# Kernel tuning notes

Measured on AMD Instinct MI355X. Metric: run time of the kernel, lower is better.

Reference implementation:

```python
import jax, jax.numpy as jnp
import numpy as np

N, E, DIN, HID, G, L = 50000, 200000, 128, 128, 64, 6
H1, H2 = 8, 4
EPS_LN, EPS_BN = 1e-5, 1e-5


def setup_inputs() -> dict:
    key = jax.random.key(0)
    ks = iter(jax.random.split(key, 32))
    def nrm(shape, scale=0.05):
        return jax.random.normal(next(ks), shape, dtype=jnp.float32) * scale
    z = lambda *s: jnp.zeros(s, jnp.float32)
    o = lambda *s: jnp.ones(s, jnp.float32)
    return {
        'x': jax.random.normal(next(ks), (N, DIN), dtype=jnp.float32),
        'edge_index': jax.random.randint(next(ks), (2, E), 0, N),
        'batch': jnp.sort(jax.random.randint(next(ks), (N,), 0, G)),
        'W1': nrm((DIN, H1 * HID)), 'a_src1': nrm((H1, HID)), 'a_dst1': nrm((H1, HID)), 'b1': z(H1 * HID),
        'W2': nrm((H1 * HID, H2 * HID)), 'a_src2': nrm((H2, HID)), 'a_dst2': nrm((H2, HID)), 'b2': z(H2 * HID),
        'W3': nrm((H2 * HID, HID)), 'b3': z(HID),
        'wq': nrm((L, HID, HID)), 'bq': z(L, HID), 'wk': nrm((L, HID, HID)), 'bk': z(L, HID),
        'wv': nrm((L, HID, HID)), 'bv': z(L, HID), 'wo': nrm((L, HID, HID)), 'bo': z(L, HID),
        'ln1g': o(L, HID), 'ln1b': z(L, HID), 'ln2g': o(L, HID), 'ln2b': z(L, HID),
        'wf1': nrm((L, HID, 4 * HID)), 'bf1': z(L, 4 * HID), 'wf2': nrm((L, 4 * HID, HID)), 'bf2': z(L, HID),
        'bn1_g': o(2 * HID), 'bn1_b': z(2 * HID),
        'fc1_w': nrm((2 * HID, HID // 2)), 'fc1_b': z(HID // 2),
        'bn2_g': o(HID // 2), 'bn2_b': z(HID // 2),
        'fc2_w': nrm((HID // 2, 2)), 'fc2_b': z(2),
    }


def _ln(x, g, b):
    mu = x.mean(-1, keepdims=True)
    v = ((x - mu) ** 2).mean(-1, keepdims=True)
    return (x - mu) * jax.lax.rsqrt(v + EPS_LN) * g + b


def _gat(x, src, dst, W, a_s, a_d, b, heads):
    # PyG GATConv: message src -> dst, segment softmax over incoming edges per dst.
    h = (x @ W).reshape(x.shape[0], heads, -1)           # [N, H, C]
    e = jax.nn.leaky_relu((h * a_s).sum(-1)[src] + (h * a_d).sum(-1)[dst], 0.2)  # [E, H]
    m = jax.ops.segment_max(e, dst, num_segments=N)
    ex = jnp.exp(e - jnp.where(jnp.isfinite(m), m, 0.0)[dst])
    s = jax.ops.segment_sum(ex, dst, num_segments=N)
    alpha = ex / (s[dst] + 1e-16)
    out = jax.ops.segment_sum(alpha[:, :, None] * h[src], dst, num_segments=N)
    return out.reshape(N, -1) + b


def _forward(x, edge_index, batch, W1, a_src1, a_dst1, b1, W2, a_src2, a_dst2, b2, W3, b3,
             wq, bq, wk, bk, wv, bv, wo, bo, ln1g, ln1b, ln2g, ln2b, wf1, bf1, wf2, bf2,
             bn1_g, bn1_b, fc1_w, fc1_b, bn2_g, bn2_b, fc2_w, fc2_b):
    loop = jnp.arange(N, dtype=edge_index.dtype)
    src = jnp.concatenate([edge_index[0], loop])          # add self-loops (PyG default)
    dst = jnp.concatenate([edge_index[1], loop])
    h = jax.nn.elu(_gat(x, src, dst, W1, a_src1, a_dst1, b1, H1))
    h = jax.nn.elu(_gat(h, src, dst, W2, a_src2, a_dst2, b2, H2))
    # GCNConv with symmetric normalization (self-loops already included)
    deg = jax.ops.segment_sum(jnp.ones(src.shape, h.dtype), dst, num_segments=N)
    dinv = jnp.where(deg > 0, jax.lax.rsqrt(jnp.maximum(deg, 1e-12)), 0.0)
    norm = dinv[src] * dinv[dst]
    h = jax.nn.elu(jax.ops.segment_sum(norm[:, None] * (h @ W3)[src], dst, num_segments=N) + b3)
    # TransformerEncoder over seq_len=1 (h3.unsqueeze(1)): softmax over one key == 1,
    # so MHA output == Wo @ (Wv h + bv) + bo exactly; q/k have no effect on the output.
    for l in range(L):
        sa = (h @ wv[l] + bv[l]) @ wo[l] + bo[l]
        h = _ln(h + sa, ln1g[l], ln1b[l])
        ff = jax.nn.gelu(h @ wf1[l] + bf1[l], approximate=False) @ wf2[l] + bf2[l]
        h = _ln(h + ff, ln2g[l], ln2b[l])
    # global mean / max pool over graphs
    cnt = jax.ops.segment_sum(jnp.ones((N,), h.dtype), batch, num_segments=G)
    hm = jax.ops.segment_sum(h, batch, num_segments=G) / jnp.maximum(cnt, 1.0)[:, None]
    hx = jax.ops.segment_max(h, batch, num_segments=G)
    hx = jnp.where(jnp.isfinite(hx), hx, 0.0)
    hc = jnp.concatenate([hm, hx], axis=1)                # [G, 2*HID]
    bn_s = 1.0 / np.sqrt(1.0 + EPS_BN)                    # eval BN: running stats (0, 1)
    hc = hc * bn_s * bn1_g + bn1_b
    hc = jax.nn.elu(hc @ fc1_w + fc1_b)
    hc = hc * bn_s * bn2_g + bn2_b
    return hc @ fc2_w + fc2_b                             # [G, 2]


def reference(x, edge_index, batch, W1, a_src1, a_dst1, b1, W2, a_src2, a_dst2, b2, W3, b3,
              wq, bq, wk, bk, wv, bv, wo, bo, ln1g, ln1b, ln2g, ln2b, wf1, bf1, wf2, bf2,
              bn1_g, bn1_b, fc1_w, fc1_b, bn2_g, bn2_b, fc2_w, fc2_b):
    return _forward(x, edge_index, batch, W1, a_src1, a_dst1, b1, W2, a_src2, a_dst2, b2, W3, b3,
                    wq, bq, wk, bk, wv, bv, wo, bo, ln1g, ln1b, ln2g, ln2b, wf1, bf1, wf2, bf2,
                    bn1_g, bn1_b, fc1_w, fc1_b, bn2_g, bn2_b, fc2_w, fc2_b)
```

## Files before the change

kernel.cpp:

```cpp
#include <hip/hip_runtime.h>
#include <hip/hip_bf16.h>
#include <math.h>

#define NN 50000
#define EE 200000
#define ET 250000
#define GG 64
#define LL 6

using short8 = __attribute__((ext_vector_type(8))) short;
using f32x4  = __attribute__((ext_vector_type(4))) float;
typedef unsigned short ushortT;

__device__ __forceinline__ float elu1(float x) { return x > 0.f ? x : expm1f(x); }
__device__ __forceinline__ float gelu_exact(float x) {
    return 0.5f * x * (1.f + erff(x * 0.70710678118654752440f));
}
__device__ __forceinline__ short f2bf(float f) {
    __hip_bfloat16 h = __float2bfloat16(f);
    return *reinterpret_cast<short*>(&h);
}
__device__ __forceinline__ float bf2f(ushortT u) {
    return __uint_as_float(((unsigned)u) << 16);
}
__device__ __forceinline__ void accum8(float* acc, float a, uint4 d) {
    acc[0] += a * bf2f((ushortT)(d.x & 0xffff));
    acc[1] += a * bf2f((ushortT)(d.x >> 16));
    acc[2] += a * bf2f((ushortT)(d.y & 0xffff));
    acc[3] += a * bf2f((ushortT)(d.y >> 16));
    acc[4] += a * bf2f((ushortT)(d.z & 0xffff));
    acc[5] += a * bf2f((ushortT)(d.z >> 16));
    acc[6] += a * bf2f((ushortT)(d.w & 0xffff));
    acc[7] += a * bf2f((ushortT)(d.w >> 16));
}

__global__ void count_deg_kernel(const int* __restrict__ ei, int* __restrict__ deg) {
    int e = blockIdx.x * 256 + threadIdx.x;
    if (e >= ET) return;
    int dst = (e < EE) ? ei[EE + e] : (e - EE);
    atomicAdd(&deg[dst], 1);
}

__global__ void scan_kernel(const int* __restrict__ deg, int* __restrict__ row_ptr, int n) {
    __shared__ int s[1024];
    int tid = threadIdx.x;
    const int per = (n + 1023) / 1024;
    int lo = tid * per, hi = min(lo + per, n);
    int sum = 0;
    for (int i = lo; i < hi; i++) sum += deg[i];
    s[tid] = sum;
    __syncthreads();
    for (int off = 1; off < 1024; off <<= 1) {
        int t = (tid >= off) ? s[tid - off] : 0;
        __syncthreads();
        s[tid] += t;
        __syncthreads();
    }
    int run = s[tid] - sum;
    for (int i = lo; i < hi; i++) { row_ptr[i] = run; run += deg[i]; }
    if (tid == 1023) row_ptr[n] = s[1023];
}

__global__ void fill_csr_kernel(const int* __restrict__ ei, const int* __restrict__ row_ptr,
                                int* __restrict__ cursor, int* __restrict__ edge_src) {
    int e = blockIdx.x * 256 + threadIdx.x;
    if (e >= ET) return;
    int src, dst;
    if (e < EE) { src = ei[e]; dst = ei[EE + e]; }
    else        { src = e - EE; dst = e - EE; }
    int pos = atomicAdd(&cursor[dst], 1);
    edge_src[row_ptr[dst] + pos] = src;
}

__global__ void dinv_kernel(const int* __restrict__ row_ptr, float* __restrict__ dinv) {
    int n = blockIdx.x * 256 + threadIdx.x;
    if (n >= NN) return;
    int d = row_ptr[n + 1] - row_ptr[n];
    dinv[n] = (d > 0) ? rsqrtf((float)d) : 0.f;
}

__global__ __launch_bounds__(256) void local_sort_kernel(
    const int* __restrict__ row_ptr, int* __restrict__ perm, int n_nodes) {
    int g = blockIdx.x * 4 + (threadIdx.x >> 6);
    int l = threadIdx.x & 63;
    int node = g * 64 + l;
    if (g * 64 >= n_nodes) return;
    int d = (node < n_nodes) ? (row_ptr[node + 1] - row_ptr[node]) : 0x7fffffff;
    int rank = 0;
#pragma unroll 16
    for (int j = 0; j < 64; j++) {
        int dj = __shfl(d, j);
        rank += (dj < d) || (dj == d && j < l);
    }
    if (node < n_nodes) perm[g * 64 + rank] = node;
}

__global__ void wvwo_kernel(const float* __restrict__ wv, const float* __restrict__ wo,
                            const float* __restrict__ bv, const float* __restrict__ bo,
                            float* __restrict__ Wvo, float* __restrict__ bvo) {
    int l = blockIdx.y;
    const float* Wv = wv + l * 16384;
    const float* Wo = wo + l * 16384;
    int tid = blockIdx.x * 256 + threadIdx.x;
    if (tid < 16384) {
        int r = tid >> 7, c = tid & 127;
        float s = 0.f;
        for (int k = 0; k < 128; k++) s += Wv[r * 128 + k] * Wo[k * 128 + c];
        Wvo[l * 16384 + tid] = s;
    }
    if (blockIdx.x == 0 && threadIdx.x < 128) {
        int c = threadIdx.x;
        float s = bo[l * 128 + c];
        for (int k = 0; k < 128; k++) s += bv[l * 128 + k] * Wo[k * 128 + c];
        bvo[l * 128 + c] = s;
    }
}

__global__ void bprep_kernel(const float* __restrict__ B, short* __restrict__ Bp,
                             int K, int N, int ldb, long srcStride) {
    int layer = blockIdx.y;
    const float* Bsrc = B + srcStride * layer;
    short* Bd = Bp + (size_t)K * N * layer;
    int total = (K >> 5) * (N >> 4) * 64;
    int tid = blockIdx.x * 256 + threadIdx.x;
    if (tid >= total) return;
    int l = tid & 63;
    int rest = tid >> 6;
    int kbc = K >> 5;
    int kb = rest % kbc;
    int c16 = rest / kbc;
    int n = c16 * 16 + (l & 15);
    int kbase = kb * 32 + (l >> 4) * 8;
    short v[8];
#pragma unroll
    for (int j = 0; j < 8; j++) v[j] = f2bf(Bsrc[(size_t)(kbase + j) * ldb + n]);
    *(uint4*)(Bd + (size_t)tid * 8) = *(uint4*)v;
}

__global__ void cast_bf16_kernel(const float* __restrict__ in, short* __restrict__ out, int n4) {
    int i = blockIdx.x * 256 + threadIdx.x;
    if (i >= n4) return;
    float4 v = *(const float4*)(in + (size_t)i * 4);
    short s[4] = { f2bf(v.x), f2bf(v.y), f2bf(v.z), f2bf(v.w) };
    *(uint2*)(out + (size_t)i * 4) = *(uint2*)s;
}

template <int EPI, bool BIAS, bool OUTBF16, int NSPLIT, int KBC,
          bool TMAJ = false, bool ATILE32 = false>
__global__ __launch_bounds__(256) void gemm_bf16_kernel(
    const short* __restrict__ A, const short* __restrict__ Bp,
    const float* __restrict__ bias, void* __restrict__ Cv,
    const float* __restrict__ a_s, const float* __restrict__ a_d,
    float* __restrict__ as_out, float* __restrict__ ad_out, int asH,
    const ushortT* __restrict__ Rres, const float* __restrict__ lng,
    const float* __restrict__ lnb, float* __restrict__ Qout,
    __hip_bfloat16* __restrict__ Qbout,
    int M, int K, int Nc) {
    __shared__ short Bs[(KBC > 0) ? KBC * 4096 : 8192];
    int t = threadIdx.x;
    int w = t >> 6, l = t & 63;
    int ln = l & 15, lq = l >> 4;
    int MBceil = (M + 63) >> 6;
    int bx = blockIdx.x;
    int xcd = bx & 7, idx = bx >> 3;
    int t2 = idx % NSPLIT;
    int mb = (idx / NSPLIT) * 8 + xcd;
    if (mb >= MBceil) return;
    int bm = mb * 64 + w * 16;
    int arow = bm + ln;
    bool aok = arow < M;
    int rowb = bm + lq * 4;
    const short* Ap = A + (size_t)arow * K + lq * 8;

    auto aload = [&](int kb) -> short8 {
        if (!aok) return (short8){0, 0, 0, 0, 0, 0, 0, 0};
        const short* p;
        if constexpr (ATILE32)
            p = A + ((size_t)kb * M + arow) * 32 + lq * 8;
        else
            p = Ap + kb * 32;
        return *(const short8*)p;
    };

    f32x4 acc[8];
#pragma unroll
    for (int j = 0; j < 8; j++) acc[j] = (f32x4){0.f, 0.f, 0.f, 0.f};

    if constexpr (KBC > 0) {
        {
            const uint4* src = (const uint4*)(Bp + (size_t)t2 * KBC * 4096);
            uint4* dst = (uint4*)Bs;
#pragma unroll
            for (int i = 0; i < KBC * 2; i++)
                dst[i * 256 + t] = src[i * 256 + t];
        }
        short8 af[KBC];
#pragma unroll
        for (int kb = 0; kb < KBC; kb++)
            af[kb] = aload(kb);
        __syncthreads();
#pragma unroll
        for (int kb = 0; kb < KBC; kb++)
#pragma unroll
            for (int ct = 0; ct < 8; ct++) {
                short8 bfr = *(const short8*)(Bs + ((ct * KBC + kb) * 64 + l) * 8);
                acc[ct] = __builtin_amdgcn_mfma_f32_16x16x32_bf16(af[kb], bfr, acc[ct], 0, 0, 0);
            }
    } else {
        int kbc = K >> 5;
        int sct = t >> 5, spart = t & 31;
        auto stage = [&](int buf, int kb) {
            const uint4* src = (const uint4*)(Bp + ((size_t)(t2 * 8 + sct) * kbc + kb) * 512);
            uint4* dst = (uint4*)(Bs + buf * 4096 + sct * 512);
            dst[spart * 2]     = src[spart * 2];
            dst[spart * 2 + 1] = src[spart * 2 + 1];
        };
        stage(0, 0);
        __syncthreads();
        for (int kb = 0; kb < kbc; kb++) {
            if (kb + 1 < kbc) stage((kb + 1) & 1, kb + 1);
            short8 af = aload(kb);
            const short* bsb = Bs + (kb & 1) * 4096;
#pragma unroll
            for (int ct = 0; ct < 8; ct++) {
                short8 bfr = *(const short8*)(bsb + (ct * 64 + l) * 8);
                acc[ct] = __builtin_amdgcn_mfma_f32_16x16x32_bf16(af, bfr, acc[ct], 0, 0, 0);
            }
            __syncthreads();
        }
    }

    if (EPI == 2) {
        const float* asv = a_s + t2 * 128;
        const float* adv = a_d + t2 * 128;
#pragma unroll
        for (int reg = 0; reg < 4; reg++) {
            float vs = 0.f, vd = 0.f;
#pragma unroll
            for (int ct = 0; ct < 8; ct++) {
                int colL = ct * 16 + ln;
                float av = acc[ct][reg];
                vs += av * asv[colL];
                vd += av * adv[colL];
            }
            vs += __shfl_xor(vs, 1); vs += __shfl_xor(vs, 2);
            vs += __shfl_xor(vs, 4); vs += __shfl_xor(vs, 8);
            vd += __shfl_xor(vd, 1); vd += __shfl_xor(vd, 2);
            vd += __shfl_xor(vd, 4); vd += __shfl_xor(vd, 8);
            int row = rowb + reg;
            if (ln == 0 && row < M) {
                as_out[(size_t)row * asH + t2] = vs;
                ad_out[(size_t)row * asH + t2] = vd;
            }
        }
    }
    if (EPI == 3) {
        float v[8][4];
#pragma unroll
        for (int ct = 0; ct < 8; ct++) {
            int col = ct * 16 + ln;
            float bv_ = bias[col];
#pragma unroll
            for (int reg = 0; reg < 4; reg++) {
                int row = rowb + reg;
                float r = (row < M) ? bf2f(Rres[(size_t)row * 128 + col]) : 0.f;
                v[ct][reg] = acc[ct][reg] + bv_ + r;
            }
        }
#pragma unroll
        for (int reg = 0; reg < 4; reg++) {
            float s = 0.f;
#pragma unroll
            for (int ct = 0; ct < 8; ct++) s += v[ct][reg];
            s += __shfl_xor(s, 1); s += __shfl_xor(s, 2);
            s += __shfl_xor(s, 4); s += __shfl_xor(s, 8);
            float mean = s * (1.f / 128.f);
            float s2 = 0.f;
#pragma unroll
            for (int ct = 0; ct < 8; ct++) { float d = v[ct][reg] - mean; s2 += d * d; }
            s2 += __shfl_xor(s2, 1); s2 += __shfl_xor(s2, 2);
            s2 += __shfl_xor(s2, 4); s2 += __shfl_xor(s2, 8);
            float rstd = rsqrtf(s2 * (1.f / 128.f) + 1e-5f);
            int row = rowb + reg;
            if (row < M) {
#pragma unroll
                for (int ct = 0; ct < 8; ct++) {
                    int col = ct * 16 + ln;
                    float o = (v[ct][reg] - mean) * rstd * lng[col] + lnb[col];
                    Qbout[(size_t)row * 128 + col] = __float2bfloat16(o);
                    if (Qout) Qout[(size_t)row * 128 + col] = o;
                }
            }
        }
    }
    if (EPI == 0 || EPI == 1 || EPI == 2) {
#pragma unroll
        for (int ct = 0; ct < 8; ct++) {
            int col = t2 * 128 + ct * 16 + ln;
            float bv_ = BIAS ? bias[col] : 0.f;
#pragma unroll
            for (int reg = 0; reg < 4; reg++) {
                int row = rowb + reg;
                if (row < M) {
                    float v = acc[ct][reg] + bv_;
                    if (EPI == 1) v = gelu_exact(v);
                    if (OUTBF16) {
                        size_t addr;
                        if constexpr (TMAJ)
                            addr = ((size_t)(col >> 5) * M + row) * 32 + (col & 31);
                        else
                            addr = (size_t)row * Nc + col;
                        ((__hip_bfloat16*)Cv)[addr] = __float2bfloat16(v);
                    } else {
                        ((float*)Cv)[(size_t)row * Nc + col] = v;
                    }
                }
            }
        }
    }
}

__global__ __launch_bounds__(256) void ff_fused_kernel(
    const short* __restrict__ Qb, const short* __restrict__ wf1p,
    const short* __restrict__ wf2p, const float* __restrict__ bf1,
    const float* __restrict__ bf2, const float* __restrict__ lng,
    const float* __restrict__ lnb, float* __restrict__ Qout,
    __hip_bfloat16* __restrict__ Qbout, int M) {
    __shared__ short Bs[16384];
    __shared__ short Ts[4][16 * 132];
    int t = threadIdx.x;
    int w = t >> 6, l = t & 63;
    int ln = l & 15, lq = l >> 4;
    int MBceil = (M + 63) >> 6;
    int bx = blockIdx.x;
    int xcd = bx & 7, mb = (bx >> 3) * 8 + xcd;
    if (mb >= MBceil) return;
    int bm = mb * 64 + w * 16;
    int arow = bm + ln;
    bool aok = arow < M;
    int rowb = bm + lq * 4;

    short8 af1[4];
#pragma unroll
    for (int kb = 0; kb < 4; kb++)
        af1[kb] = aok ? *(const short8*)(Qb + (size_t)arow * 128 + kb * 32 + lq * 8)
                      : (short8){0, 0, 0, 0, 0, 0, 0, 0};

    f32x4 acc2[8];
#pragma unroll
    for (int j = 0; j < 8; j++) acc2[j] = (f32x4){0.f, 0.f, 0.f, 0.f};

    short* Tw = &Ts[w][0];
    for (int kc = 0; kc < 4; kc++) {
        __syncthreads();
        {
            const uint4* src = (const uint4*)(wf1p + kc * 16384);
            uint4* dst = (uint4*)Bs;
#pragma unroll
            for (int i = 0; i < 8; i++) dst[i * 256 + t] = src[i * 256 + t];
        }
        __syncthreads();
        f32x4 acct[8];
#pragma unroll
        for (int j = 0; j < 8; j++) acct[j] = (f32x4){0.f, 0.f, 0.f, 0.f};
#pragma unroll
        for (int kb = 0; kb < 4; kb++)
#pragma unroll
            for (int ct = 0; ct < 8; ct++) {
                short8 bfr = *(const short8*)(Bs + ((ct * 4 + kb) * 64 + l) * 8);
                acct[ct] = __builtin_amdgcn_mfma_f32_16x16x32_bf16(af1[kb], bfr, acct[ct], 0, 0, 0);
            }
#pragma unroll
        for (int ct = 0; ct < 8; ct++) {
            float bv = bf1[kc * 128 + ct * 16 + ln];
#pragma unroll
            for (int reg = 0; reg < 4; reg++)
                Tw[(lq * 4 + reg) * 132 + ct * 16 + ln] = f2bf(gelu_exact(acct[ct][reg] + bv));
        }
        __syncthreads();
        {
            int sct = t >> 5, spart = t & 31;
            const uint4* src = (const uint4*)(wf2p + (size_t)(sct * 16 + kc * 4) * 512);
            uint4* dst = (uint4*)Bs + sct * 256;
#pragma unroll
            for (int j = 0; j < 8; j++) dst[spart + j * 32] = src[spart + j * 32];
        }
        short8 a2[4];
#pragma unroll
        for (int kb2 = 0; kb2 < 4; kb2++)
            a2[kb2] = *(const short8*)(Tw + ln * 132 + kb2 * 32 + lq * 8);
        __syncthreads();
#pragma unroll
        for (int kb2 = 0; kb2 < 4; kb2++)
#pragma unroll
            for (int ct = 0; ct < 8; ct++) {
                short8 bfr = *(const short8*)(Bs + ((ct * 4 + kb2) * 64 + l) * 8);
                acc2[ct] = __builtin_amdgcn_mfma_f32_16x16x32_bf16(a2[kb2], bfr, acc2[ct], 0, 0, 0);
            }
    }

    float v[8][4];
#pragma unroll
    for (int ct = 0; ct < 8; ct++) {
        int col = ct * 16 + ln;
        float bv_ = bf2[col];
#pragma unroll
        for (int reg = 0; reg < 4; reg++) {
            int row = rowb + reg;
            float r = (row < M) ? bf2f(((const ushortT*)Qb)[(size_t)row * 128 + col]) : 0.f;
            v[ct][reg] = acc2[ct][reg] + bv_ + r;
        }
    }
#pragma unroll
    for (int reg = 0; reg < 4; reg++) {
        float s = 0.f;
#pragma unroll
        for (int ct = 0; ct < 8; ct++) s += v[ct][reg];
        s += __shfl_xor(s, 1); s += __shfl_xor(s, 2);
        s += __shfl_xor(s, 4); s += __shfl_xor(s, 8);
        float mean = s * (1.f / 128.f);
        float s2 = 0.f;
#pragma unroll
        for (int ct = 0; ct < 8; ct++) { float d = v[ct][reg] - mean; s2 += d * d; }
        s2 += __shfl_xor(s2, 1); s2 += __shfl_xor(s2, 2);
        s2 += __shfl_xor(s2, 4); s2 += __shfl_xor(s2, 8);
        float rstd = rsqrtf(s2 * (1.f / 128.f) + 1e-5f);
        int row = rowb + reg;
        if (row < M) {
#pragma unroll
            for (int ct = 0; ct < 8; ct++) {
                int col = ct * 16 + ln;
                float o = (v[ct][reg] - mean) * rstd * lng[col] + lnb[col];
                Qbout[(size_t)row * 128 + col] = __float2bfloat16(o);
                if (Qout) Qout[(size_t)row * 128 + col] = o;
            }
        }
    }
}

template <int H>
__global__ __launch_bounds__(256) void gat_alpha_kernel(
    const float* __restrict__ as_, const float* __restrict__ ad_,
    const int* __restrict__ row_ptr, const int* __restrict__ edge_src,
    float* __restrict__ exA, float* __restrict__ exS, int n_nodes) {
    const int GS = 64 / H;
    int node = blockIdx.x * 4 + (threadIdx.x >> 6);
    if (node >= n_nodes) return;
    int l = threadIdx.x & 63;
    int h = l / GS;
    int lig = l % GS;
    int start = row_ptr[node];
    int deg = row_ptr[node + 1] - start;
    float adn = ad_[(size_t)node * H + h];
    float m = -1e30f;
    for (int j = lig; j < deg; j += GS) {
        int s = edge_src[start + j];
        float e = as_[(size_t)s * H + h] + adn;
        e = e > 0.f ? e : 0.2f * e;
        m = fmaxf(m, e);
    }
#pragma unroll
    for (int mask = 1; mask < GS; mask <<= 1)
        m = fmaxf(m, __shfl_xor(m, mask));
    float S = 0.f;
    for (int j = lig; j < deg; j += GS) {
        int s = edge_src[start + j];
        float e = as_[(size_t)s * H + h] + adn;
        e = e > 0.f ? e : 0.2f * e;
        float ex = expf(e - m);
        exA[(size_t)h * ET + (start + j)] = ex;
        S += ex;
    }
#pragma unroll
    for (int mask = 1; mask < GS; mask <<= 1)
        S += __shfl_xor(S, mask);
    if (lig == 0) exS[(size_t)h * n_nodes + node] = S;
}

__global__ __launch_bounds__(256) void gat_agg_tiled_kernel(
    const ushortT* __restrict__ hT, const float* __restrict__ exA,
    const float* __restrict__ exS, const float* __restrict__ bias,
    const int* __restrict__ row_ptr, const int* __restrict__ edge_src,
    const int* __restrict__ perm,
    __hip_bfloat16* __restrict__ outT, int n_nodes, int NB) {
    int bx = blockIdx.x;
    int xcd = bx & 7, rest = bx >> 3;
    int tl = rest / NB, nb = rest - tl * NB;
    int tile = tl * 8 + xcd;
    int nl = threadIdx.x >> 2, q = threadIdx.x & 3;
    int idx = nb * 64 + nl;
    if (idx >= n_nodes) return;
    int node = perm[idx];
    int hb = tile >> 2;
    const ushortT* __restrict__ base = hT + (size_t)tile * n_nodes * 32 + q * 8;
    const float* __restrict__ exAh = exA + (size_t)hb * ET;
    int start = row_ptr[node];
    int deg = row_ptr[node + 1] - start;
    float acc[8];
#pragma unroll
    for (int c = 0; c < 8; c++) acc[c] = 0.f;
    for (int j = 0; j < deg; j++) {
        int s = edge_src[start + j];
        float a = exAh[start + j];
        uint4 d = *(const uint4*)(base + (size_t)s * 32);
        accum8(acc, a, d);
    }
    float inv = 1.f / (exS[(size_t)hb * n_nodes + node] + 1e-16f);
    const float* bp = bias + tile * 32 + q * 8;
    short o[8];
#pragma unroll
    for (int c = 0; c < 8; c++)
        o[c] = f2bf(elu1(acc[c] * inv + bp[c]));
    *(uint4*)(outT + ((size_t)tile * n_nodes + node) * 32 + q * 8) = *(uint4*)o;
}

__global__ __launch_bounds__(256, 2) void gcn_agg_kernel(
    const ushortT* __restrict__ hp, const float* __restrict__ dinv,
    const float* __restrict__ b3, const int* __restrict__ row_ptr,
    const int* __restrict__ edge_src,
    __hip_bfloat16* __restrict__ outb, int n_nodes) {
    int node = blockIdx.x * 2 + (threadIdx.x >> 7);
    int c = threadIdx.x & 127;
    if (node >= n_nodes) return;
    int start = row_ptr[node];
    int deg = row_ptr[node + 1] - start;
    float dn = dinv[node];
    float acc = 0.f;
    auto LS = [&](int j) { return edge_src[start + min(j, deg - 1)]; };
    int s0 = LS(0), s1 = LS(1), s2 = LS(2), s3 = LS(3);
    int s4 = LS(4), s5 = LS(5), s6 = LS(6), s7 = LS(7);
    auto HW = [&](int s, int j, float& h, float& w) {
        h = bf2f(hp[(size_t)s * 128 + c]);
        w = (j < deg) ? dinv[s] * dn : 0.f;
    };
    float h0, h1, h2, h3, h4, h5, h6, h7;
    float w0, w1, w2, w3, w4, w5, w6, w7;
    HW(s0, 0, h0, w0); HW(s1, 1, h1, w1); HW(s2, 2, h2, w2); HW(s3, 3, h3, w3);
    HW(s4, 4, h4, w4); HW(s5, 5, h5, w5); HW(s6, 6, h6, w6); HW(s7, 7, h7, w7);
    int j0 = 0;
    while (true) {
        int jn = j0 + 8;
        bool more = jn < deg;
        float g0, g1, g2, g3, g4, g5, g6, g7;
        float v0 = 0.f, v1 = 0.f, v2 = 0.f, v3 = 0.f;
        float v4 = 0.f, v5 = 0.f, v6 = 0.f, v7 = 0.f;
        if (more) {
            int t0 = LS(jn),     t1 = LS(jn + 1), t2 = LS(jn + 2), t3 = LS(jn + 3);
            int t4 = LS(jn + 4), t5 = LS(jn + 5), t6 = LS(jn + 6), t7 = LS(jn + 7);
            HW(t0, jn,     g0, v0); HW(t1, jn + 1, g1, v1);
            HW(t2, jn + 2, g2, v2); HW(t3, jn + 3, g3, v3);
            HW(t4, jn + 4, g4, v4); HW(t5, jn + 5, g5, v5);
            HW(t6, jn + 6, g6, v6); HW(t7, jn + 7, g7, v7);
        }
        acc += w0 * h0 + w1 * h1 + w2 * h2 + w3 * h3
             + w4 * h4 + w5 * h5 + w6 * h6 + w7 * h7;
        if (!more) break;
        h0 = g0; h1 = g1; h2 = g2; h3 = g3;
        h4 = g4; h5 = g5; h6 = g6; h7 = g7;
        w0 = v0; w1 = v1; w2 = v2; w3 = v3;
        w4 = v4; w5 = v5; w6 = v6; w7 = v7;
        j0 = jn;
    }
    outb[(size_t)node * 128 + c] = __float2bfloat16(elu1(acc + b3[c]));
}

__global__ void pool1_kernel(const float* __restrict__ Q, const int* __restrict__ batch,
                             float* __restrict__ psum, float* __restrict__ pmax, int n_nodes) {
    int g = blockIdx.x, seg = blockIdx.y;
    int c = threadIdx.x;
    int lo, hi;
    {
        int l = 0, h = n_nodes;
        while (l < h) { int mid = (l + h) >> 1; if (batch[mid] < g) l = mid + 1; else h = mid; }
        lo = l;
        l = lo; h = n_nodes;
        while (l < h) { int mid = (l + h) >> 1; if (batch[mid] < g + 1) l = mid + 1; else h = mid; }
        hi = l;
    }
    int len = hi - lo;
    int a = lo + (int)((long)len * seg / 8);
    int b = lo + (int)((long)len * (seg + 1) / 8);
    float s = 0.f, mx = -INFINITY;
    for (int n = a; n < b; n++) {
        float v = Q[(size_t)n * 128 + c];
        s += v;
        mx = fmaxf(mx, v);
    }
    psum[(g * 8 + seg) * 128 + c] = s;
    pmax[(g * 8 + seg) * 128 + c] = mx;
}

__global__ void pool2_kernel(const float* __restrict__ psum, const float* __restrict__ pmax,
                             const int* __restrict__ batch,
                             const float* __restrict__ bn1g, const float* __restrict__ bn1b,
                             float* __restrict__ hc, int n_nodes) {
    int g = blockIdx.x;
    int c = threadIdx.x;
    int lo, hi;
    {
        int l = 0, h = n_nodes;
        while (l < h) { int mid = (l + h) >> 1; if (batch[mid] < g) l = mid + 1; else h = mid; }
        lo = l;
        l = lo; h = n_nodes;
        while (l < h) { int mid = (l + h) >> 1; if (batch[mid] < g + 1) l = mid + 1; else h = mid; }
        hi = l;
    }
    int cnt = hi - lo;
    float s = 0.f, mx = -INFINITY;
    for (int seg = 0; seg < 8; seg++) {
        s += psum[(g * 8 + seg) * 128 + c];
        mx = fmaxf(mx, pmax[(g * 8 + seg) * 128 + c]);
    }
    float hm = s / fmaxf((float)cnt, 1.f);
    float hx = (cnt > 0 && isfinite(mx)) ? mx : 0.f;
    const float bn_s = 0.99999500003749968f;
    hc[g * 256 + c]       = hm * bn_s * bn1g[c] + bn1b[c];
    hc[g * 256 + 128 + c] = hx * bn_s * bn1g[128 + c] + bn1b[128 + c];
}

__global__ void head_kernel(const float* __restrict__ hc,
                            const float* __restrict__ fc1w, const float* __restrict__ fc1b,
                            const float* __restrict__ bn2g, const float* __restrict__ bn2b,
                            const float* __restrict__ fc2w, const float* __restrict__ fc2b,
                            float* __restrict__ out) {
    int g = blockIdx.x;
    int j = threadIdx.x;
    const float bn_s = 0.99999500003749968f;
    float acc = fc1b[j];
    for (int i = 0; i < 256; i++) acc += hc[g * 256 + i] * fc1w[i * 64 + j];
    acc = elu1(acc);
    acc = acc * bn_s * bn2g[j] + bn2b[j];
    __shared__ float sv[64];
    sv[j] = acc;
    __syncthreads();
    if (j < 2) {
        float o = fc2b[j];
        for (int i = 0; i < 64; i++) o += sv[i] * fc2w[i * 2 + j];
        out[g * 2 + j] = o;
    }
}

extern "C" void kernel_launch(void* const* d_in, const int* in_sizes, int n_in,
                              void* d_out, int out_size, void* d_ws, size_t ws_size,
                              hipStream_t stream) {
    const float* x    = (const float*)d_in[0];
    const int*   ei   = (const int*)d_in[1];
    const int*   batch= (const int*)d_in[2];
    const float* W1   = (const float*)d_in[3];
    const float* as1  = (const float*)d_in[4];
    const float* ad1  = (const float*)d_in[5];
    const float* b1   = (const float*)d_in[6];
    const float* W2   = (const float*)d_in[7];
    const float* as2  = (const float*)d_in[8];
    const float* ad2  = (const float*)d_in[9];
    const float* b2   = (const float*)d_in[10];
    const float* W3   = (const float*)d_in[11];
    const float* b3   = (const float*)d_in[12];
    const float* wv   = (const float*)d_in[17];
    const float* bv   = (const float*)d_in[18];
    const float* wo   = (const float*)d_in[19];
    const float* bo   = (const float*)d_in[20];
    const float* ln1g = (const float*)d_in[21];
    const float* ln1b = (const float*)d_in[22];
    const float* ln2g = (const float*)d_in[23];
    const float* ln2b = (const float*)d_in[24];
    const float* wf1  = (const float*)d_in[25];
    const float* bf1  = (const float*)d_in[26];
    const float* wf2  = (const float*)d_in[27];
    const float* bf2  = (const float*)d_in[28];
    const float* bn1g = (const float*)d_in[29];
    const float* bn1b = (const float*)d_in[30];
    const float* fc1w = (const float*)d_in[31];
    const float* fc1b = (const float*)d_in[32];
    const float* bn2g = (const float*)d_in[33];
    const float* bn2b = (const float*)d_in[34];
    const float* fc2w = (const float*)d_in[35];
    const float* fc2b = (const float*)d_in[36];
    float* out = (float*)d_out;

    char* wsb = (char*)d_ws;
    short* xb    = (short*)wsb;
    float* exAf  = (float*)wsb;
    float* exSf  = (float*)(wsb + 8000000);
    short* h1t   = (short*)(wsb + 12800000);
    short* h2t   = (short*)(wsb + 12800000);
    short* h3pre = (short*)(wsb + 12800000);
    short* bh1   = (short*)(wsb + 115200000);
    short* bh2   = (short*)(wsb + 115200000);
    float* fQ    = (float*)(wsb + 128000000);
    short* Qb    = (short*)(wsb + 153600000);
    char* tail = wsb + 217600000;
    short* W1p  = (short*)tail;  tail += 262144;
    short* W2p  = (short*)tail;  tail += 1048576;
    short* W3p  = (short*)tail;  tail += 131072;
    short* Wvop = (short*)tail;  tail += 196608;
    short* wf1p = (short*)tail;  tail += 786432;
    short* wf2p = (short*)tail;  tail += 786432;
    float* Wvo  = (float*)tail;  tail += 393216;
    float* bvo  = (float*)tail;  tail += 3072;
    float* fAS  = (float*)tail;  tail += 1600000;
    float* fAD  = (float*)tail;  tail += 1600000;
    float* fDv  = (float*)tail;  tail += 200000;
    float* psum = (float*)tail;  tail += 262144;
    float* pmax = (float*)tail;  tail += 262144;
    float* fHC  = (float*)tail;  tail += 65536;
    int* iDeg   = (int*)tail;    tail += 200000;
    int* iRP    = (int*)tail;    tail += 200004;
    int* iCur   = (int*)tail;    tail += 200000;
    int* iES    = (int*)tail;    tail += 1000000;

    hipMemsetAsync(iDeg, 0, NN * sizeof(int), stream);
    hipMemsetAsync(iCur, 0, NN * sizeof(int), stream);

    count_deg_kernel<<<(ET + 255) / 256, 256, 0, stream>>>(ei, iDeg);
    scan_kernel<<<1, 1024, 0, stream>>>(iDeg, iRP, NN);
    fill_csr_kernel<<<(ET + 255) / 256, 256, 0, stream>>>(ei, iRP, iCur, iES);
    dinv_kernel<<<(NN + 255) / 256, 256, 0, stream>>>(iRP, fDv);
    int* perm = iCur;
    local_sort_kernel<<<(NN / 64 + 4) / 4, 256, 0, stream>>>(iRP, perm, NN);

    wvwo_kernel<<<dim3(64, 6), 256, 0, stream>>>(wv, wo, bv, bo, Wvo, bvo);
    auto bprep = [&](const float* B, short* Bp, int K, int N, int ldb, long sStride, int layers) {
        int total = (K >> 5) * (N >> 4) * 64;
        dim3 grid((total + 255) / 256, layers);
        bprep_kernel<<<grid, 256, 0, stream>>>(B, Bp, K, N, ldb, sStride);
    };
    bprep(W1, W1p, 128, 1024, 1024, 0, 1);
    bprep(W2, W2p, 1024, 512, 512, 0, 1);
    bprep(W3, W3p, 512, 128, 128, 0, 1);
    bprep(Wvo, Wvop, 128, 128, 128, 16384, 6);
    bprep(wf1, wf1p, 128, 512, 512, 65536, 6);
    bprep(wf2, wf2p, 512, 128, 128, 65536, 6);
    cast_bf16_kernel<<<(NN * 128 / 4 + 255) / 256, 256, 0, stream>>>(x, xb, NN * 128 / 4);

    const int MB64 = (NN + 63) / 64;
    const int MBp = ((MB64 + 7) / 8) * 8;
    const int NB = (NN + 63) / 64;

    gemm_bf16_kernel<2, false, true, 8, 4, true, false><<<MBp * 8, 256, 0, stream>>>(
        xb, W1p, nullptr, h1t, as1, ad1, fAS, fAD, 8,
        nullptr, nullptr, nullptr, nullptr, nullptr, NN, 128, 1024);
    gat_alpha_kernel<8><<<(NN + 3) / 4, 256, 0, stream>>>(
        fAS, fAD, iRP, iES, exAf, exSf, NN);
    gat_agg_tiled_kernel<<<4 * NB * 8, 256, 0, stream>>>(
        (const ushortT*)h1t, exAf, exSf, b1, iRP, iES, perm, (__hip_bfloat16*)bh1, NN, NB);
    gemm_bf16_kernel<2, false, true, 4, 0, true, true><<<MBp * 4, 256, 0, stream>>>(
        bh1, W2p, nullptr, h2t, as2, ad2, fAS, fAD, 4,
        nullptr, nullptr, nullptr, nullptr, nullptr, NN, 1024, 512);
    gat_alpha_kernel<4><<<(NN + 3) / 4, 256, 0, stream>>>(
        fAS, fAD, iRP, iES, exAf, exSf, NN);
    gat_agg_tiled_kernel<<<2 * NB * 8, 256, 0, stream>>>(
        (const ushortT*)h2t, exAf, exSf, b2, iRP, iES, perm, (__hip_bfloat16*)bh2, NN, NB);
    gemm_bf16_kernel<0, false, true, 1, 0, false, true><<<MBp, 256, 0, stream>>>(
        bh2, W3p, nullptr, h3pre, nullptr, nullptr, nullptr, nullptr, 0,
        nullptr, nullptr, nullptr, nullptr, nullptr, NN, 512, 128);
    gcn_agg_kernel<<<(NN + 1) / 2, 256, 0, stream>>>(
        (const ushortT*)h3pre, fDv, b3, iRP, iES, (__hip_bfloat16*)Qb, NN);
    for (int l = 0; l < LL; l++) {
        gemm_bf16_kernel<3, true, false, 1, 4><<<MBp, 256, 0, stream>>>(
            Qb, Wvop + l * 16384, bvo + l * 128, nullptr, nullptr, nullptr, nullptr, nullptr, 0,
            (const ushortT*)Qb, ln1g + l * 128, ln1b + l * 128, nullptr, (__hip_bfloat16*)Qb,
            NN, 128, 128);
        ff_fused_kernel<<<MBp, 256, 0, stream>>>(
            Qb, wf1p + l * 65536, wf2p + l * 65536, bf1 + l * 512, bf2 + l * 128,
            ln2g + l * 128, ln2b + l * 128,
            (l == LL - 1) ? fQ : nullptr, (__hip_bfloat16*)Qb, NN);
    }
    pool1_kernel<<<dim3(GG, 8), 128, 0, stream>>>(fQ, batch, psum, pmax, NN);
    pool2_kernel<<<GG, 128, 0, stream>>>(psum, pmax, batch, bn1g, bn1b, fHC, NN);
    head_kernel<<<GG, 64, 0, stream>>>(fHC, fc1w, fc1b, bn2g, bn2b, fc2w, fc2b, out);
}
```

Before: 1.331 ms.

## Fuse all six transformer layers into one persistent per-row-tile kernel

Replaces the 12 per-layer launches (V/O GEMM with residual+LN, then fused FFN with residual+LN) with a single kernel. Each block keeps its 64-row activation tile in registers as bf16 across all layers and reshapes it into MFMA operands through LDS, so the Q activations are not re-read from and re-written to global memory between layers. The final layer's fp32 output is written directly. Weights are still streamed from global memory into shared memory for every layer. Occupancy may drop because of the added register pressure and the longer per-block work.

```diff
diff --git a/kernel.cpp b/kernel.cpp
--- a/kernel.cpp
+++ b/kernel.cpp
@@ -152,9 +152,6 @@
     const float* __restrict__ bias, void* __restrict__ Cv,
     const float* __restrict__ a_s, const float* __restrict__ a_d,
     float* __restrict__ as_out, float* __restrict__ ad_out, int asH,
-    const ushortT* __restrict__ Rres, const float* __restrict__ lng,
-    const float* __restrict__ lnb, float* __restrict__ Qout,
-    __hip_bfloat16* __restrict__ Qbout,
     int M, int K, int Nc) {
     __shared__ short Bs[(KBC > 0) ? KBC * 4096 : 8192];
     int t = threadIdx.x;
@@ -254,80 +251,40 @@
             }
         }
     }
-    if (EPI == 3) {
-        float v[8][4];
-#pragma unroll
-        for (int ct = 0; ct < 8; ct++) {
-            int col = ct * 16 + ln;
-            float bv_ = bias[col];
-#pragma unroll
-            for (int reg = 0; reg < 4; reg++) {
-                int row = rowb + reg;
-                float r = (row < M) ? bf2f(Rres[(size_t)row * 128 + col]) : 0.f;
-                v[ct][reg] = acc[ct][reg] + bv_ + r;
-            }
-        }
+#pragma unroll
+    for (int ct = 0; ct < 8; ct++) {
+        int col = t2 * 128 + ct * 16 + ln;
+        float bv_ = BIAS ? bias[col] : 0.f;
 #pragma unroll
         for (int reg = 0; reg < 4; reg++) {
-            float s = 0.f;
-#pragma unroll
-            for (int ct = 0; ct < 8; ct++) s += v[ct][reg];
-            s += __shfl_xor(s, 1); s += __shfl_xor(s, 2);
-            s += __shfl_xor(s, 4); s += __shfl_xor(s, 8);
-            float mean = s * (1.f / 128.f);
-            float s2 = 0.f;
-#pragma unroll
-            for (int ct = 0; ct < 8; ct++) { float d = v[ct][reg] - mean; s2 += d * d; }
-            s2 += __shfl_xor(s2, 1); s2 += __shfl_xor(s2, 2);
-            s2 += __shfl_xor(s2, 4); s2 += __shfl_xor(s2, 8);
-            float rstd = rsqrtf(s2 * (1.f / 128.f) + 1e-5f);
             int row = rowb + reg;
             if (row < M) {
-#pragma unroll
-                for (int ct = 0; ct < 8; ct++) {
-                    int col = ct * 16 + ln;
-                    float o = (v[ct][reg] - mean) * rstd * lng[col] + lnb[col];
-                    Qbout[(size_t)row * 128 + col] = __float2bfloat16(o);
-                    if (Qout) Qout[(size_t)row * 128 + col] = o;
+                float v = acc[ct][reg] + bv_;
+                if (OUTBF16) {
+                    size_t addr;
+                    if constexpr (TMAJ)
+                        addr = ((size_t)(col >> 5) * M + row) * 32 + (col & 31);
+                    else
+                        addr = (size_t)row * Nc + col;
+                    ((__hip_bfloat16*)Cv)[addr] = __float2bfloat16(v);
+                } else {
+                    ((float*)Cv)[(size_t)row * Nc + col] = v;
                 }
             }
         }
     }
-    if (EPI == 0 || EPI == 1 || EPI == 2) {
-#pragma unroll
-        for (int ct = 0; ct < 8; ct++) {
-            int col = t2 * 128 + ct * 16 + ln;
-            float bv_ = BIAS ? bias[col] : 0.f;
-#pragma unroll
-            for (int reg = 0; reg < 4; reg++) {
-                int row = rowb + reg;
-                if (row < M) {
-                    float v = acc[ct][reg] + bv_;
-                    if (EPI == 1) v = gelu_exact(v);
-                    if (OUTBF16) {
-                        size_t addr;
-                        if constexpr (TMAJ)
-                            addr = ((size_t)(col >> 5) * M + row) * 32 + (col & 31);
-                        else
-                            addr = (size_t)row * Nc + col;
-                        ((__hip_bfloat16*)Cv)[addr] = __float2bfloat16(v);
-                    } else {
-                        ((float*)Cv)[(size_t)row * Nc + col] = v;
-                    }
-                }
-            }
-        }
-    }
-}
-
-__global__ __launch_bounds__(256) void ff_fused_kernel(
-    const short* __restrict__ Qb, const short* __restrict__ wf1p,
+}
+
+#define TS 136
+__global__ __launch_bounds__(256) void transformer_fused_kernel(
+    const short* __restrict__ Qb, const short* __restrict__ Wvop,
+    const float* __restrict__ bvo, const short* __restrict__ wf1p,
     const short* __restrict__ wf2p, const float* __restrict__ bf1,
-    const float* __restrict__ bf2, const float* __restrict__ lng,
-    const float* __restrict__ lnb, float* __restrict__ Qout,
-    __hip_bfloat16* __restrict__ Qbout, int M) {
+    const float* __restrict__ bf2, const float* __restrict__ ln1g,
+    const float* __restrict__ ln1b, const float* __restrict__ ln2g,
+    const float* __restrict__ ln2b, float* __restrict__ fQ, int M) {
     __shared__ short Bs[16384];
-    __shared__ short Ts[4][16 * 132];
+    __shared__ short Ts[4][16 * TS];
     int t = threadIdx.x;
     int w = t >> 6, l = t & 63;
     int ln = l & 15, lq = l >> 4;
@@ -336,105 +293,143 @@
     int xcd = bx & 7, mb = (bx >> 3) * 8 + xcd;
     if (mb >= MBceil) return;
     int bm = mb * 64 + w * 16;
-    int arow = bm + ln;
-    bool aok = arow < M;
     int rowb = bm + lq * 4;
-
-    short8 af1[4];
-#pragma unroll
-    for (int kb = 0; kb < 4; kb++)
-        af1[kb] = aok ? *(const short8*)(Qb + (size_t)arow * 128 + kb * 32 + lq * 8)
-                      : (short8){0, 0, 0, 0, 0, 0, 0, 0};
-
-    f32x4 acc2[8];
-#pragma unroll
-    for (int j = 0; j < 8; j++) acc2[j] = (f32x4){0.f, 0.f, 0.f, 0.f};
-
     short* Tw = &Ts[w][0];
-    for (int kc = 0; kc < 4; kc++) {
+
+    ushortT hc[8][4];
+#pragma unroll
+    for (int ct = 0; ct < 8; ct++) {
+        int col = ct * 16 + ln;
+#pragma unroll
+        for (int reg = 0; reg < 4; reg++) {
+            int row = rowb + reg;
+            hc[ct][reg] = (row < M) ? ((const ushortT*)Qb)[(size_t)row * 128 + col] : 0;
+        }
+    }
+
+    auto bounceA = [&](short8* a) {
+#pragma unroll
+        for (int ct = 0; ct < 8; ct++)
+#pragma unroll
+            for (int reg = 0; reg < 4; reg++)
+                Tw[(lq * 4 + reg) * TS + ct * 16 + ln] = (short)hc[ct][reg];
+#pragma unroll
+        for (int kb = 0; kb < 4; kb++)
+            a[kb] = *(const short8*)(Tw + ln * TS + kb * 32 + lq * 8);
+    };
+    auto lnEpi = [&](f32x4* acc, const float* bias, const float* g,
+                     const float* b, bool writeF) {
+        float v[8][4];
+#pragma unroll
+        for (int ct = 0; ct < 8; ct++) {
+            float bv_ = bias[ct * 16 + ln];
+#pragma unroll
+            for (int reg = 0; reg < 4; reg++)
+                v[ct][reg] = acc[ct][reg] + bv_ + bf2f(hc[ct][reg]);
+        }
+#pragma unroll
+        for (int reg = 0; reg < 4; reg++) {
+            float s = 0.f;
+#pragma unroll
+            for (int ct = 0; ct < 8; ct++) s += v[ct][reg];
+            s += __shfl_xor(s, 1); s += __shfl_xor(s, 2);
+            s += __shfl_xor(s, 4); s += __shfl_xor(s, 8);
+            float mean = s * (1.f / 128.f);
+            float s2 = 0.f;
+#pragma unroll
+            for (int ct = 0; ct < 8; ct++) { float d = v[ct][reg] - mean; s2 += d * d; }
+            s2 += __shfl_xor(s2, 1); s2 += __shfl_xor(s2, 2);
+            s2 += __shfl_xor(s2, 4); s2 += __shfl_xor(s2, 8);
+            float rstd = rsqrtf(s2 * (1.f / 128.f) + 1e-5f);
+            int row = rowb + reg;
+#pragma unroll
+            for (int ct = 0; ct < 8; ct++) {
+                int col = ct * 16 + ln;
+                float o = (v[ct][reg] - mean) * rstd * g[col] + b[col];
+                hc[ct][reg] = (ushortT)f2bf(o);
+                if (writeF && row < M) fQ[(size_t)row * 128 + col] = o;
+            }
+        }
+    };
+
+    for (int lay = 0; lay < LL; lay++) {
+        short8 a1[4];
+        bounceA(a1);
         __syncthreads();
         {
-            const uint4* src = (const uint4*)(wf1p + kc * 16384);
+            const uint4* src = (const uint4*)(Wvop + (size_t)lay * 16384);
             uint4* dst = (uint4*)Bs;
 #pragma unroll
             for (int i = 0; i < 8; i++) dst[i * 256 + t] = src[i * 256 + t];
         }
         __syncthreads();
-        f32x4 acct[8];
-#pragma unroll
-        for (int j = 0; j < 8; j++) acct[j] = (f32x4){0.f, 0.f, 0.f, 0.f};
+        f32x4 acc1[8];
+#pragma unroll
+        for (int j = 0; j < 8; j++) acc1[j] = (f32x4){0.f, 0.f, 0.f, 0.f};
 #pragma unroll
         for (int kb = 0; kb < 4; kb++)
 #pragma unroll
             for (int ct = 0; ct < 8; ct++) {
                 short8 bfr = *(const short8*)(Bs + ((ct * 4 + kb) * 64 + l) * 8);
-                acct[ct] = __builtin_amdgcn_mfma_f32_16x16x32_bf16(af1[kb], bfr, acct[ct], 0, 0, 0);
-            }
-#pragma unroll
-        for (int ct = 0; ct < 8; ct++) {
-            float bv = bf1[kc * 128 + ct * 16 + ln];
-#pragma unroll
-            for (int reg = 0; reg < 4; reg++)
-                Tw[(lq * 4 + reg) * 132 + ct * 16 + ln] = f2bf(gelu_exact(acct[ct][reg] + bv));
-        }
-        __syncthreads();
-        {
-            int sct = t >> 5, spart = t & 31;
-            const uint4* src = (const uint4*)(wf2p + (size_t)(sct * 16 + kc * 4) * 512);
-            uint4* dst = (uint4*)Bs + sct * 256;
-#pragma unroll
-            for (int j = 0; j < 8; j++) dst[spart + j * 32] = src[spart + j * 32];
-        }
-        short8 a2[4];
-#pragma unroll
-        for (int kb2 = 0; kb2 < 4; kb2++)
-            a2[kb2] = *(const short8*)(Tw + ln * 132 + kb2 * 32 + lq * 8);
-        __syncthreads();
-#pragma unroll
-        for (int kb2 = 0; kb2 < 4; kb2++)
+                acc1[ct] = __builtin_amdgcn_mfma_f32_16x16x32_bf16(a1[kb], bfr, acc1[ct], 0, 0, 0);
+            }
+        lnEpi(acc1, bvo + lay * 128, ln1g + lay * 128, ln1b + lay * 128, false);
+
+        short8 af1[4];
+        bounceA(af1);
+        const short* w1l = wf1p + (size_t)lay * 65536;
+        const short* w2l = wf2p + (size_t)lay * 65536;
+        f32x4 acc2[8];
+#pragma unroll
+        for (int j = 0; j < 8; j++) acc2[j] = (f32x4){0.f, 0.f, 0.f, 0.f};
+        for (int kc = 0; kc < 4; kc++) {
+            __syncthreads();
+            {
+                const uint4* src = (const uint4*)(w1l + kc * 16384);
+                uint4* dst = (uint4*)Bs;
+#pragma unroll
+                for (int i = 0; i < 8; i++) dst[i * 256 + t] = src[i * 256 + t];
+            }
+            __syncthreads();
+            f32x4 acct[8];
+#pragma unroll
+            for (int j = 0; j < 8; j++) acct[j] = (f32x4){0.f, 0.f, 0.f, 0.f};
+#pragma unroll
+            for (int kb = 0; kb < 4; kb++)
+#pragma unroll
+                for (int ct = 0; ct < 8; ct++) {
+                    short8 bfr = *(const short8*)(Bs + ((ct * 4 + kb) * 64 + l) * 8);
+                    acct[ct] = __builtin_amdgcn_mfma_f32_16x16x32_bf16(af1[kb], bfr, acct[ct], 0, 0, 0);
+                }
 #pragma unroll
             for (int ct = 0; ct < 8; ct++) {
-                short8 bfr = *(const short8*)(Bs + ((ct * 4 + kb2) * 64 + l) * 8);
-                acc2[ct] = __builtin_amdgcn_mfma_f32_16x16x32_bf16(a2[kb2], bfr, acc2[ct], 0, 0, 0);
-            }
-    }
-
-    float v[8][4];
-#pragma unroll
-    for (int ct = 0; ct < 8; ct++) {
-        int col = ct * 16 + ln;
-        float bv_ = bf2[col];
-#pragma unroll
-        for (int reg = 0; reg < 4; reg++) {
-            int row = rowb + reg;
-            float r = (row < M) ? bf2f(((const ushortT*)Qb)[(size_t)row * 128 + col]) : 0.f;
-            v[ct][reg] = acc2[ct][reg] + bv_ + r;
-        }
-    }
-#pragma unroll
-    for (int reg = 0; reg < 4; reg++) {
-        float s = 0.f;
-#pragma unroll
-        for (int ct = 0; ct < 8; ct++) s += v[ct][reg];
-        s += __shfl_xor(s, 1); s += __shfl_xor(s, 2);
-        s += __shfl_xor(s, 4); s += __shfl_xor(s, 8);
-        float mean = s * (1.f / 128.f);
-        float s2 = 0.f;
-#pragma unroll
-        for (int ct = 0; ct < 8; ct++) { float d = v[ct][reg] - mean; s2 += d * d; }
-        s2 += __shfl_xor(s2, 1); s2 += __shfl_xor(s2, 2);
-        s2 += __shfl_xor(s2, 4); s2 += __shfl_xor(s2, 8);
-        float rstd = rsqrtf(s2 * (1.f / 128.f) + 1e-5f);
-        int row = rowb + reg;
-        if (row < M) {
-#pragma unroll
-            for (int ct = 0; ct < 8; ct++) {
-                int col = ct * 16 + ln;
-                float o = (v[ct][reg] - mean) * rstd * lng[col] + lnb[col];
-                Qbout[(size_t)row * 128 + col] = __float2bfloat16(o);
-                if (Qout) Qout[(size_t)row * 128 + col] = o;
-            }
-        }
+                float bv = bf1[lay * 512 + kc * 128 + ct * 16 + ln];
+#pragma unroll
+                for (int reg = 0; reg < 4; reg++)
+                    Tw[(lq * 4 + reg) * TS + ct * 16 + ln] = f2bf(gelu_exact(acct[ct][reg] + bv));
+            }
+            short8 a2[4];
+#pragma unroll
+            for (int kb2 = 0; kb2 < 4; kb2++)
+                a2[kb2] = *(const short8*)(Tw + ln * TS + kb2 * 32 + lq * 8);
+            __syncthreads();
+            {
+                int sct = t >> 5, spart = t & 31;
+                const uint4* src = (const uint4*)(w2l + (size_t)(sct * 16 + kc * 4) * 512);
+                uint4* dst = (uint4*)Bs + sct * 256;
+#pragma unroll
+                for (int j = 0; j < 8; j++) dst[spart + j * 32] = src[spart + j * 32];
+            }
+            __syncthreads();
+#pragma unroll
+            for (int kb2 = 0; kb2 < 4; kb2++)
+#pragma unroll
+                for (int ct = 0; ct < 8; ct++) {
+                    short8 bfr = *(const short8*)(Bs + ((ct * 4 + kb2) * 64 + l) * 8);
+                    acc2[ct] = __builtin_amdgcn_mfma_f32_16x16x32_bf16(a2[kb2], bfr, acc2[ct], 0, 0, 0);
+                }
+        }
+        lnEpi(acc2, bf2 + lay * 128, ln2g + lay * 128, ln2b + lay * 128, lay == LL - 1);
     }
 }
 
@@ -738,34 +733,23 @@
     const int NB = (NN + 63) / 64;
 
     gemm_bf16_kernel<2, false, true, 8, 4, true, false><<<MBp * 8, 256, 0, stream>>>(
-        xb, W1p, nullptr, h1t, as1, ad1, fAS, fAD, 8,
-        nullptr, nullptr, nullptr, nullptr, nullptr, NN, 128, 1024);
+        xb, W1p, nullptr, h1t, as1, ad1, fAS, fAD, 8, NN, 128, 1024);
     gat_alpha_kernel<8><<<(NN + 3) / 4, 256, 0, stream>>>(
         fAS, fAD, iRP, iES, exAf, exSf, NN);
     gat_agg_tiled_kernel<<<4 * NB * 8, 256, 0, stream>>>(
         (const ushortT*)h1t, exAf, exSf, b1, iRP, iES, perm, (__hip_bfloat16*)bh1, NN, NB);
     gemm_bf16_kernel<2, false, true, 4, 0, true, true><<<MBp * 4, 256, 0, stream>>>(
-        bh1, W2p, nullptr, h2t, as2, ad2, fAS, fAD, 4,
-        nullptr, nullptr, nullptr, nullptr, nullptr, NN, 1024, 512);
+        bh1, W2p, nullptr, h2t, as2, ad2, fAS, fAD, 4, NN, 1024, 512);
     gat_alpha_kernel<4><<<(NN + 3) / 4, 256, 0, stream>>>(
         fAS, fAD, iRP, iES, exAf, exSf, NN);
     gat_agg_tiled_kernel<<<2 * NB * 8, 256, 0, stream>>>(
         (const ushortT*)h2t, exAf, exSf, b2, iRP, iES, perm, (__hip_bfloat16*)bh2, NN, NB);
     gemm_bf16_kernel<0, false, true, 1, 0, false, true><<<MBp, 256, 0, stream>>>(
-        bh2, W3p, nullptr, h3pre, nullptr, nullptr, nullptr, nullptr, 0,
-        nullptr, nullptr, nullptr, nullptr, nullptr, NN, 512, 128);
+        bh2, W3p, nullptr, h3pre, nullptr, nullptr, nullptr, nullptr, 0, NN, 512, 128);
     gcn_agg_kernel<<<(NN + 1) / 2, 256, 0, stream>>>(
         (const ushortT*)h3pre, fDv, b3, iRP, iES, (__hip_bfloat16*)Qb, NN);
-    for (int l = 0; l < LL; l++) {
-        gemm_bf16_kernel<3, true, false, 1, 4><<<MBp, 256, 0, stream>>>(
-            Qb, Wvop + l * 16384, bvo + l * 128, nullptr, nullptr, nullptr, nullptr, nullptr, 0,
-            (const ushortT*)Qb, ln1g + l * 128, ln1b + l * 128, nullptr, (__hip_bfloat16*)Qb,
-            NN, 128, 128);
-        ff_fused_kernel<<<MBp, 256, 0, stream>>>(
-            Qb, wf1p + l * 65536, wf2p + l * 65536, bf1 + l * 512, bf2 + l * 128,
-            ln2g + l * 128, ln2b + l * 128,
-            (l == LL - 1) ? fQ : nullptr, (__hip_bfloat16*)Qb, NN);
-    }
+    transformer_fused_kernel<<<MBp, 256, 0, stream>>>(
+        Qb, Wvop, bvo, wf1p, wf2p, bf1, bf2, ln1g, ln1b, ln2g, ln2b, fQ, NN);
     pool1_kernel<<<dim3(GG, 8), 128, 0, stream>>>(fQ, batch, psum, pmax, NN);
     pool2_kernel<<<GG, 128, 0, stream>>>(psum, pmax, batch, bn1g, bn1b, fHC, NN);
     head_kernel<<<GG, 64, 0, stream>>>(fHC, fc1w, fc1b, bn2g, bn2b, fc2w, fc2b, out);
```

Result: faster. 1.111 ms (-16.5%).
